# Optimization experiments

Measured on AMD Instinct MI355X. Metric: run time of the kernel, lower is better.

Reference implementation:

```python
import jax, jax.numpy as jnp
import numpy as np


def _uniform_directions(key, num_thetas, d):
    # dect.generate_uniform_directions: gaussian columns normalized to unit norm, shape [d, T]
    v = jax.random.normal(key, (d, num_thetas), dtype=jnp.float32)
    return v / jnp.linalg.norm(v, axis=0, keepdims=True)


def _compute_ect(x, v, radius, resolution, scale):
    # x: [N, d], v: [d, T] -> nh: [N, T] projections of points onto directions
    nh = x @ v
    # thresholds: [R, 1, 1]
    lin = jnp.linspace(-radius, radius, resolution, dtype=x.dtype)[:, None, None]
    # scaled sigmoid of (threshold - projection), broadcast to [R, N, T]
    ecc = jax.nn.sigmoid(scale * (lin - nh))
    # Euler characteristic curve: sum over points -> [R, T]
    return ecc.sum(axis=1)


def setup_inputs() -> dict:
    key = jax.random.key(0)
    k1, k2 = jax.random.split(key)
    space1 = jax.random.normal(k1, (384, 128), dtype=jnp.float32)
    space2 = jax.random.normal(k2, (384, 32), dtype=jnp.float32)
    return {"space1": space1, "space2": space2}


def reference(space1, space2):
    n1, d1 = space1.shape
    n2, d2 = space2.shape
    RADIUS = 1.0
    SCALE = 500.0
    # directions generated deterministically (seed 42 in original) per space dims
    v1 = _uniform_directions(jax.random.key(42), n1, d1)
    v2 = _uniform_directions(jax.random.key(42), n2, d2)
    input_ect = _compute_ect(space1, v1, RADIUS, n1, SCALE)   # [n1, n1]
    latent_ect = _compute_ect(space2, v2, RADIUS, n2, SCALE)  # [n2, n2]
    # MSELoss (mean reduction)
    loss = jnp.mean((input_ect - latent_ect) ** 2)
    return loss
```

## Files before the change

### kernel.cpp

```cpp
#include <hip/hip_runtime.h>
#include <hip/hip_bf16.h>
#include <stdint.h>

#define TT 384
#define NN 384
#define RR 384
#define D1 128
#define D2 32

#define THETA 0.0352f
#define HALF_SLOTS 191.5f
#define BAND_ITERS 14

__device__ inline void threefry2x32(uint32_t k0, uint32_t k1,
                                    uint32_t x0, uint32_t x1,
                                    uint32_t& o0, uint32_t& o1) {
    uint32_t ks2 = k0 ^ k1 ^ 0x1BD11BDAu;
    x0 += k0; x1 += k1;
    #define TF_ROUND(r) { x0 += x1; x1 = (x1 << (r)) | (x1 >> (32 - (r))); x1 ^= x0; }
    TF_ROUND(13) TF_ROUND(15) TF_ROUND(26) TF_ROUND(6)
    x0 += k1;  x1 += ks2 + 1u;
    TF_ROUND(17) TF_ROUND(29) TF_ROUND(16) TF_ROUND(24)
    x0 += ks2; x1 += k0 + 2u;
    TF_ROUND(13) TF_ROUND(15) TF_ROUND(26) TF_ROUND(6)
    x0 += k0;  x1 += k1 + 3u;
    TF_ROUND(17) TF_ROUND(29) TF_ROUND(16) TF_ROUND(24)
    x0 += k1;  x1 += ks2 + 4u;
    TF_ROUND(13) TF_ROUND(15) TF_ROUND(26) TF_ROUND(6)
    x0 += ks2; x1 += k0 + 5u;
    #undef TF_ROUND
    o0 = x0; o1 = x1;
}

__device__ inline float erfinv_f32(float x) {
    float w = -log1pf(-x * x);
    float p;
    if (w < 5.0f) {
        w = w - 2.5f;
        p =            2.81022636e-08f;
        p = fmaf(p, w, 3.43273939e-07f);
        p = fmaf(p, w, -3.5233877e-06f);
        p = fmaf(p, w, -4.39150654e-06f);
        p = fmaf(p, w, 0.00021858087f);
        p = fmaf(p, w, -0.00125372503f);
        p = fmaf(p, w, -0.00417768164f);
        p = fmaf(p, w, 0.246640727f);
        p = fmaf(p, w, 1.50140941f);
    } else {
        w = sqrtf(w) - 3.0f;
        p =            -0.000200214257f;
        p = fmaf(p, w, 0.000100950558f);
        p = fmaf(p, w, 0.00134934322f);
        p = fmaf(p, w, -0.00367342844f);
        p = fmaf(p, w, 0.00573950773f);
        p = fmaf(p, w, -0.0076224613f);
        p = fmaf(p, w, 0.00943887047f);
        p = fmaf(p, w, 1.00167406f);
        p = fmaf(p, w, 2.83297682f);
    }
    return p * x;
}

__device__ inline float bits_to_normal(uint32_t bits) {
    uint32_t fb = (bits >> 9) | 0x3F800000u;
    float f = __uint_as_float(fb) - 1.0f;
    float lo = __uint_as_float(0xBF7FFFFFu);
    float u = f * 2.0f + lo;
    u = fmaxf(lo, u);
    return 1.41421356237f * erfinv_f32(u);
}

__global__ void gen_dirs_all(float* __restrict__ v1, float* __restrict__ v2,
                             float* __restrict__ out) {
    int bid = blockIdx.x;
    int i = threadIdx.x;
    if (bid == 0 && i == 0) out[0] = 0.0f;
    int j, d; float* v;
    if (bid < TT) { j = bid;      d = D1; v = v1; }
    else          { j = bid - TT; d = D2; v = v2; }
    __shared__ float sh[128];
    float val = 0.0f;
    if (i < d) {
        uint32_t flat = (uint32_t)i * TT + (uint32_t)j;
        uint32_t o0, o1;
        threefry2x32(0u, 42u, 0u, flat, o0, o1);
        val = bits_to_normal(o0 ^ o1);
    }
    sh[i] = val * val;
    __syncthreads();
    for (int s = 64; s > 0; s >>= 1) {
        if (i < s) sh[i] += sh[i + s];
        __syncthreads();
    }
    float nrm = sqrtf(sh[0]);
    if (i < d) v[i * TT + j] = val / nrm;
}

template<int D>
__device__ inline void proj_body(float* __restrict__ nh, const float* __restrict__ x,
                                 const float* __restrict__ v, int t, int n) {
    const float* xr = x + n * D;
    float acc = 0.0f;
    #pragma unroll 16
    for (int k = 0; k < D; ++k)
        acc = fmaf(xr[k], v[k * TT + t], acc);
    nh[n * TT + t] = acc;
}

__global__ void proj_all(float* __restrict__ nh1, float* __restrict__ nh2,
                         const float* __restrict__ x1, const float* __restrict__ x2,
                         const float* __restrict__ v1, const float* __restrict__ v2) {
    int t = blockIdx.x * 128 + threadIdx.x;
    int n = blockIdx.y;
    if (blockIdx.z == 0) proj_body<D1>(nh1, x1, v1, t, n);
    else                 proj_body<D2>(nh2, x2, v2, t, n);
}

__device__ inline void scatter_point(float p, float sgn,
                                     float* __restrict__ inc,
                                     float* __restrict__ band) {
    int r1  = (int)ceilf((p + (1.0f + THETA)) * HALF_SLOTS);
    int rlo = (int)ceilf((p + (1.0f - THETA)) * HALF_SLOTS);
    if (r1 <= 0)        atomicAdd(&inc[0], sgn);
    else if (r1 <= 383) atomicAdd(&inc[r1], sgn);
    #pragma unroll
    for (int j = 0; j < BAND_ITERS; ++j) {
        int r = rlo + j;
        if (r >= 0 && r < r1 && r < RR) {
            float lin = -1.0f + 2.0f * (float)r / 383.0f;
            float sig = __builtin_amdgcn_rcpf(1.0f + __expf(500.0f * (p - lin)));
            atomicAdd(&band[r], sgn * sig);
        }
    }
}

__global__ void __launch_bounds__(384) ect_loss_kernel(
        const float* __restrict__ nh1, const float* __restrict__ nh2,
        float* __restrict__ out) {
    int t = blockIdx.x;
    int tid = threadIdx.x;
    __shared__ float inc[RR];
    __shared__ float band[RR];
    __shared__ float red[6];
    inc[tid] = 0.0f;
    band[tid] = 0.0f;
    __syncthreads();

    float p1 = nh1[tid * TT + t];
    float p2 = nh2[tid * TT + t];
    scatter_point(p1,  1.0f, inc, band);
    scatter_point(p2, -1.0f, inc, band);
    __syncthreads();

    for (int s = 1; s < RR; s <<= 1) {
        float v = inc[tid];
        if (tid >= s) v += inc[tid - s];
        __syncthreads();
        inc[tid] = v;
        __syncthreads();
    }

    float d = inc[tid] + band[tid];
    float sq = d * d;
    #pragma unroll
    for (int off = 32; off > 0; off >>= 1)
        sq += __shfl_xor(sq, off, 64);
    if ((tid & 63) == 0) red[tid >> 6] = sq;
    __syncthreads();
    if (tid == 0) {
        float s = red[0] + red[1] + red[2] + red[3] + red[4] + red[5];
        atomicAdd(out, s * (1.0f / ((float)RR * (float)TT)));
    }
}

extern "C" void kernel_launch(void* const* d_in, const int* in_sizes, int n_in,
                              void* d_out, int out_size, void* d_ws, size_t ws_size,
                              hipStream_t stream) {
    const float* space1 = (const float*)d_in[0];
    const float* space2 = (const float*)d_in[1];
    float* out = (float*)d_out;

    float* ws = (float*)d_ws;
    float* v1  = ws;
    float* v2  = v1 + D1 * TT;
    float* nh1 = v2 + D2 * TT;
    float* nh2 = nh1 + NN * TT;

    gen_dirs_all<<<2 * TT, 128, 0, stream>>>(v1, v2, out);
    proj_all<<<dim3(TT / 128, NN, 2), 128, 0, stream>>>(nh1, nh2, space1, space2, v1, v2);
    ect_loss_kernel<<<TT, 384, 0, stream>>>(nh1, nh2, out);
}
```

Measured before the change: 87.62 us.

## Fuse direction generation and projection into ECT kernel, use wave-shuffle scan

Direction generation and the point projection are moved into the per-direction ECT kernel: each block generates its own direction vector in shared memory and computes projections directly from transposed inputs produced by a small prep kernel. This removes two launches and the global round-trip of the projection matrix. The shared-memory Hillis-Steele prefix sum is replaced by a wave-level shuffle scan plus per-wave offsets, which cuts the number of barriers. In exchange, each block rereads the whole input (cached), and a transpose prep kernel is added.

```diff
diff --git a/kernel.cpp b/kernel.cpp
--- a/kernel.cpp
+++ b/kernel.cpp
@@ -70,50 +70,21 @@
     return 1.41421356237f * erfinv_f32(u);
 }
 
-__global__ void gen_dirs_all(float* __restrict__ v1, float* __restrict__ v2,
-                             float* __restrict__ out) {
-    int bid = blockIdx.x;
-    int i = threadIdx.x;
-    if (bid == 0 && i == 0) out[0] = 0.0f;
-    int j, d; float* v;
-    if (bid < TT) { j = bid;      d = D1; v = v1; }
-    else          { j = bid - TT; d = D2; v = v2; }
-    __shared__ float sh[128];
-    float val = 0.0f;
-    if (i < d) {
-        uint32_t flat = (uint32_t)i * TT + (uint32_t)j;
-        uint32_t o0, o1;
-        threefry2x32(0u, 42u, 0u, flat, o0, o1);
-        val = bits_to_normal(o0 ^ o1);
+__global__ void prep_kernel(float* __restrict__ xT1, float* __restrict__ xT2,
+                            const float* __restrict__ x1, const float* __restrict__ x2,
+                            float* __restrict__ out) {
+    int idx = blockIdx.x * 256 + threadIdx.x;
+    if (idx == 0) out[0] = 0.0f;
+    if (idx < D1 * TT) {
+        int k = idx / NN, n = idx % NN;
+        xT1[idx] = x1[n * D1 + k];
+    } else {
+        int idx2 = idx - D1 * TT;
+        if (idx2 < D2 * TT) {
+            int k = idx2 / NN, n = idx2 % NN;
+            xT2[idx2] = x2[n * D2 + k];
+        }
     }
-    sh[i] = val * val;
-    __syncthreads();
-    for (int s = 64; s > 0; s >>= 1) {
-        if (i < s) sh[i] += sh[i + s];
-        __syncthreads();
-    }
-    float nrm = sqrtf(sh[0]);
-    if (i < d) v[i * TT + j] = val / nrm;
-}
-
-template<int D>
-__device__ inline void proj_body(float* __restrict__ nh, const float* __restrict__ x,
-                                 const float* __restrict__ v, int t, int n) {
-    const float* xr = x + n * D;
-    float acc = 0.0f;
-    #pragma unroll 16
-    for (int k = 0; k < D; ++k)
-        acc = fmaf(xr[k], v[k * TT + t], acc);
-    nh[n * TT + t] = acc;
-}
-
-__global__ void proj_all(float* __restrict__ nh1, float* __restrict__ nh2,
-                         const float* __restrict__ x1, const float* __restrict__ x2,
-                         const float* __restrict__ v1, const float* __restrict__ v2) {
-    int t = blockIdx.x * 128 + threadIdx.x;
-    int n = blockIdx.y;
-    if (blockIdx.z == 0) proj_body<D1>(nh1, x1, v1, t, n);
-    else                 proj_body<D2>(nh2, x2, v2, t, n);
 }
 
 __device__ inline void scatter_point(float p, float sgn,
@@ -134,38 +105,69 @@
     }
 }
 
-__global__ void __launch_bounds__(384) ect_loss_kernel(
-        const float* __restrict__ nh1, const float* __restrict__ nh2,
+__global__ void __launch_bounds__(384) ect_fused(
+        const float* __restrict__ xT1, const float* __restrict__ xT2,
         float* __restrict__ out) {
     int t = blockIdx.x;
     int tid = threadIdx.x;
+    int lane = tid & 63;
+    int w = tid >> 6;
+    __shared__ float v1s[D1];
+    __shared__ float v2s[D2];
     __shared__ float inc[RR];
     __shared__ float band[RR];
-    __shared__ float red[6];
+    __shared__ float red[8];
+
+    float g = 0.0f;
+    if (tid < D1 + D2) {
+        int i = (tid < D1) ? tid : tid - D1;
+        uint32_t flat = (uint32_t)i * TT + (uint32_t)t;
+        uint32_t o0, o1;
+        threefry2x32(0u, 42u, 0u, flat, o0, o1);
+        g = bits_to_normal(o0 ^ o1);
+    }
+    float sq = g * g;
+    #pragma unroll
+    for (int off = 32; off > 0; off >>= 1) sq += __shfl_xor(sq, off, 64);
+    if (lane == 0) red[w] = sq;
+    __syncthreads();
+    float nrm1 = sqrtf(red[0] + red[1]);
+    float nrm2 = sqrtf(red[2]);
+    if (tid < D1)           v1s[tid] = g / nrm1;
+    else if (tid < D1 + D2) v2s[tid - D1] = g / nrm2;
     inc[tid] = 0.0f;
     band[tid] = 0.0f;
     __syncthreads();
 
-    float p1 = nh1[tid * TT + t];
-    float p2 = nh2[tid * TT + t];
+    int n = tid;
+    float p1 = 0.0f, p2 = 0.0f;
+    #pragma unroll 8
+    for (int k = 0; k < D1; ++k) p1 = fmaf(xT1[k * NN + n], v1s[k], p1);
+    #pragma unroll 8
+    for (int k = 0; k < D2; ++k) p2 = fmaf(xT2[k * NN + n], v2s[k], p2);
+
     scatter_point(p1,  1.0f, inc, band);
     scatter_point(p2, -1.0f, inc, band);
     __syncthreads();
 
-    for (int s = 1; s < RR; s <<= 1) {
-        float v = inc[tid];
-        if (tid >= s) v += inc[tid - s];
-        __syncthreads();
-        inc[tid] = v;
-        __syncthreads();
+    float v = inc[tid];
+    #pragma unroll
+    for (int s = 1; s < 64; s <<= 1) {
+        float u = __shfl_up(v, s, 64);
+        if (lane >= s) v += u;
     }
+    if (lane == 63) red[w] = v;
+    __syncthreads();
+    float off_acc = 0.0f;
+    for (int j = 0; j < w; ++j) off_acc += red[j];
+    v += off_acc;
 
-    float d = inc[tid] + band[tid];
-    float sq = d * d;
+    float d = v + band[tid];
+    float s2 = d * d;
     #pragma unroll
-    for (int off = 32; off > 0; off >>= 1)
-        sq += __shfl_xor(sq, off, 64);
-    if ((tid & 63) == 0) red[tid >> 6] = sq;
+    for (int off = 32; off > 0; off >>= 1) s2 += __shfl_xor(s2, off, 64);
+    __syncthreads();
+    if (lane == 0) red[w] = s2;
     __syncthreads();
     if (tid == 0) {
         float s = red[0] + red[1] + red[2] + red[3] + red[4] + red[5];
@@ -181,12 +183,9 @@
     float* out = (float*)d_out;
 
     float* ws = (float*)d_ws;
-    float* v1  = ws;
-    float* v2  = v1 + D1 * TT;
-    float* nh1 = v2 + D2 * TT;
-    float* nh2 = nh1 + NN * TT;
+    float* xT1 = ws;
+    float* xT2 = xT1 + D1 * TT;
 
-    gen_dirs_all<<<2 * TT, 128, 0, stream>>>(v1, v2, out);
-    proj_all<<<dim3(TT / 128, NN, 2), 128, 0, stream>>>(nh1, nh2, space1, space2, v1, v2);
-    ect_loss_kernel<<<TT, 384, 0, stream>>>(nh1, nh2, out);
+    prep_kernel<<<240, 256, 0, stream>>>(xT1, xT2, space1, space2, out);
+    ect_fused<<<TT, 384, 0, stream>>>(xT1, xT2, out);
 }
```

Measured after the change: 86.70 us. Within noise of the previous version (-1.0%).
